# Kernel tuning notes

Measured on AMD Instinct MI355X. Metric: run time of the kernel, lower is better.

The kernel has to match this reference:

```python
import jax, jax.numpy as jnp
import numpy as np

DIM = 1024
LATENT_DIM = 512
NUM_HEADS = 16
HEAD_DIM = DIM // NUM_HEADS
SCALE = HEAD_DIM ** -0.5


def setup_inputs() -> dict:
    key = jax.random.key(0)
    k1, k2, k3, k4, k5 = jax.random.split(key, 5)
    B, xN, zN = 2, 2048, 2048
    x = jax.random.normal(k1, (B, xN, DIM), dtype=jnp.float32)
    z = jax.random.normal(k2, (B, zN, LATENT_DIM), dtype=jnp.float32)
    # torch Linear weights: [out_features, in_features]
    Wq = jax.random.normal(k3, (DIM, DIM), dtype=jnp.float32) * (DIM ** -0.5)
    Wkv = jax.random.normal(k4, (2 * DIM, LATENT_DIM), dtype=jnp.float32) * (LATENT_DIM ** -0.5)
    Wo = jax.random.normal(k5, (DIM, DIM), dtype=jnp.float32) * (DIM ** -0.5)
    return {"x": x, "z": z, "Wq": Wq, "Wkv": Wkv, "Wo": Wo}


def reference(x, z, Wq, Wkv, Wo):
    B, xN, _ = x.shape
    _, zN, _ = z.shape
    # projections (torch Linear: y = x @ W.T)
    Q = (x @ Wq.T).reshape(B, xN, NUM_HEADS, HEAD_DIM)        # [B,xN,H,D]
    KV = (z @ Wkv.T).reshape(B, zN, 2, NUM_HEADS, HEAD_DIM)   # [B,zN,2,H,D]
    K = KV[:, :, 0]                                            # [B,zN,H,D]
    V = KV[:, :, 1]
    attn = jnp.einsum('bqhd,bkhd->bhqk', Q, K) * SCALE         # [B,H,xN,zN]
    attn = jax.nn.softmax(attn, axis=-1)
    O = jnp.einsum('bhqk,bkhd->bqhd', attn, V).reshape(B, xN, DIM)
    return O @ Wo.T
```

## Files before the change

kernel.cpp:

```cpp
#include <hip/hip_runtime.h>
#include <stdint.h>

#define SEQ 2048
#define QSCALE 0.1803368801111244f
#define DEFER_THR 11.5f

typedef __attribute__((ext_vector_type(8))) short bf16x8;
typedef __attribute__((ext_vector_type(4))) short bf16x4;
typedef __attribute__((ext_vector_type(4))) float f32x4;
typedef __attribute__((ext_vector_type(16))) float f32x16;
typedef unsigned short u16;

__device__ __forceinline__ u16 f2bf(float f) {
  union { float f; uint32_t u; } v; v.f = f;
  uint32_t u = v.u;
  u += 0x7fffu + ((u >> 16) & 1u);
  return (u16)(u >> 16);
}

__device__ __forceinline__ float fast_exp2(float x) {
#if __has_builtin(__builtin_amdgcn_exp2f)
  return __builtin_amdgcn_exp2f(x);
#else
  return exp2f(x);
#endif
}

__device__ __forceinline__ uint32_t cvtpk(float a, float b) {
  uint32_t r;
  asm("v_cvt_pk_bf16_f32 %0, %1, %2" : "=v"(r) : "v"(a), "v"(b));
  return r;
}

__device__ __forceinline__ void swap_pair(uint32_t& a, uint32_t& b, int hi) {
  uint32_t ta = (uint32_t)__shfl_xor((int)a, 32);
  uint32_t tb = (uint32_t)__shfl_xor((int)b, 32);
  a = hi ? tb : a;
  b = hi ? b : ta;
}

__device__ __forceinline__ void gload_lds16(const u16* g, u16* l) {
  __builtin_amdgcn_global_load_lds((__attribute__((address_space(1))) void*)g,
                                   (__attribute__((address_space(3))) void*)l,
                                   16, 0, 0);
}

__global__ void cvt5_kernel(const float* __restrict__ x, const float* __restrict__ z,
                            const float* __restrict__ Wq, const float* __restrict__ Wkv,
                            const float* __restrict__ Wo,
                            u16* __restrict__ xb, u16* __restrict__ zb,
                            u16* __restrict__ wqb, u16* __restrict__ wkvb,
                            u16* __restrict__ wob) {
  const int X4 = 1048576, Z4 = 524288, W4 = 262144;
  const int total = X4 + Z4 + 3 * W4;
  int i = blockIdx.x * blockDim.x + threadIdx.x;
  const int stride = gridDim.x * blockDim.x;
  for (; i < total; i += stride) {
    const float* src; u16* dst; int j = i;
    if (j < X4)              { src = x;   dst = xb; }
    else if ((j -= X4) < Z4) { src = z;   dst = zb; }
    else if ((j -= Z4) < W4) { src = Wq;  dst = wqb; }
    else if ((j -= W4) < W4) { src = Wkv; dst = wkvb; }
    else       { j -= W4;      src = Wo;  dst = wob; }
    float4 v = ((const float4*)src)[j];
    bf16x4 o;
    o[0] = (short)f2bf(v.x); o[1] = (short)f2bf(v.y);
    o[2] = (short)f2bf(v.z); o[3] = (short)f2bf(v.w);
    ((bf16x4*)dst)[j] = o;
  }
}

template <int BN, typename CT>
__device__ __forceinline__ void gemm_bt_body(const u16* __restrict__ A,
                                             const u16* __restrict__ B,
                                             CT* __restrict__ C,
                                             int N, int K, float scale,
                                             int tm, int tn, u16* As, u16* Bs) {
  constexpr int NB = BN / 32;
  constexpr int NBG = BN / 64;
  const int tid = threadIdx.x;
  const int wid = tid >> 6;
  const int lane = tid & 63;
  const int lg = lane >> 4, lq = lane & 15;
  const int wr = wid >> 1, wc = wid & 1;

  f32x4 acc[4][NB];
#pragma unroll
  for (int m = 0; m < 4; m++)
#pragma unroll
    for (int n = 0; n < NB; n++)
#pragma unroll
      for (int e = 0; e < 4; e++) acc[m][n][e] = 0.f;

  const int r0 = tid >> 2;
  const int s0 = tid & 3;
  const int sc = (s0 ^ ((r0 >> 1) & 3)) * 8;
  const u16* gA0 = A + (size_t)(tm * 128 + r0) * K + sc;
  const u16* gA1 = gA0 + (size_t)64 * K;
  const u16* gB0 = B + (size_t)(tn * BN + r0) * K + sc;
  const u16* gB1 = gB0 + (size_t)64 * K;
  u16* lA = As + wid * 512;
  u16* lB = Bs + wid * 512;

  const int rslot = (lg ^ ((lq >> 1) & 3)) * 8;

  for (int k0 = 0; k0 < K; k0 += 32) {
    __syncthreads();
    gload_lds16(gA0 + k0, lA);
    gload_lds16(gA1 + k0, lA + 2048);
    gload_lds16(gB0 + k0, lB);
    if constexpr (NBG == 2) gload_lds16(gB1 + k0, lB + 2048);
    __syncthreads();

    bf16x8 af[4], bfr[NB];
#pragma unroll
    for (int m = 0; m < 4; m++)
      af[m] = *(const bf16x8*)(As + (wr * 64 + m * 16 + lq) * 32 + rslot);
#pragma unroll
    for (int n = 0; n < NB; n++)
      bfr[n] = *(const bf16x8*)(Bs + (wc * (BN / 2) + n * 16 + lq) * 32 + rslot);
#pragma unroll
    for (int m = 0; m < 4; m++)
#pragma unroll
      for (int n = 0; n < NB; n++)
        acc[m][n] = __builtin_amdgcn_mfma_f32_16x16x32_bf16(af[m], bfr[n], acc[m][n], 0, 0, 0);
  }

#pragma unroll
  for (int m = 0; m < 4; m++) {
    const int row = tm * 128 + wr * 64 + m * 16 + lg * 4;
#pragma unroll
    for (int i = 0; i < 4; i++) {
      CT* cp = C + (size_t)(row + i) * N + tn * BN + wc * (BN / 2) + lq;
#pragma unroll
      for (int n = 0; n < NB; n++) {
        float v = acc[m][n][i] * scale;
        if constexpr (sizeof(CT) == 2) cp[n * 16] = (CT)f2bf(v);
        else                            cp[n * 16] = (CT)v;
      }
    }
  }
}

__global__ __launch_bounds__(256) void qkv_gemm(const u16* __restrict__ xb,
                                                const u16* __restrict__ zb,
                                                const u16* __restrict__ Wqb,
                                                const u16* __restrict__ Wkvb,
                                                u16* __restrict__ Qb,
                                                u16* __restrict__ Kb,
                                                u16* __restrict__ VTb) {
  __shared__ __align__(16) u16 As[128 * 32];
  __shared__ __align__(16) u16 Bs[128 * 32];
  int g = blockIdx.x;
  if (g < 256) {
    gemm_bt_body<128, u16>(xb, Wqb, Qb, 1024, 1024, QSCALE, g >> 3, g & 7, As, Bs);
  } else if (g < 512) {
    g -= 256;
    gemm_bt_body<128, u16>(zb, Wkvb, Kb, 1024, 512, 1.f, g >> 3, g & 7, As, Bs);
  } else {
    g -= 512;
    gemm_bt_body<128, u16>(Wkvb + 1024 * 512, zb, VTb, 4096, 512, 1.f, g >> 5, g & 31, As, Bs);
  }
}

__global__ __launch_bounds__(256) void o_gemm(const u16* __restrict__ Ob,
                                              const u16* __restrict__ Wob,
                                              float* __restrict__ out) {
  __shared__ __align__(16) u16 As[128 * 32];
  __shared__ __align__(16) u16 Bs[64 * 32];
  gemm_bt_body<64, float>(Ob, Wob, out, 1024, 1024, 1.f, blockIdx.y, blockIdx.x, As, Bs);
}

__global__ __launch_bounds__(256, 4) void attn_kernel(const u16* __restrict__ Q,
                                                      const u16* __restrict__ K,
                                                      const u16* __restrict__ VT,
                                                      u16* __restrict__ OP,
                                                      float2* __restrict__ ml) {
  __shared__ __align__(16) u16 LDS[16384];

  const int tid = threadIdx.x;
  const int wid = tid >> 6;
  const int lane = tid & 63;
  const int l31 = lane & 31;
  const int hi = lane >> 5;

  const int bi = blockIdx.x;
  const int xcd = bi & 7, j = bi >> 3;
  const int qt = j & 15;
  const int s  = (j >> 4) & 1;
  const int bh = xcd + 8 * (j >> 5);
  const int b = bh >> 4, h = bh & 15;
  const int t0 = s * 16;

  const int q0 = qt * 128 + wid * 32;

  bf16x8 qf[4];
  {
    const u16* qp = Q + (size_t)(b * SEQ + q0 + l31) * 1024 + h * 64 + hi * 8;
#pragma unroll
    for (int ks = 0; ks < 4; ks++) qf[ks] = *(const bf16x8*)(qp + ks * 16);
  }

  f32x16 of[2];
#pragma unroll
  for (int d = 0; d < 2; d++)
#pragma unroll
    for (int e = 0; e < 16; e++) of[d][e] = 0.f;
  float m_run = -3.0e38f, l_run = 0.f;

  const char* rdB[4];
#pragma unroll
  for (int ks = 0; ks < 4; ks++)
    rdB[ks] = (const char*)LDS + l31 * 128 + ((((2 * ks + hi) ^ (lane & 7))) << 4);

  const int r0 = tid >> 3;
  const int srcc = ((tid & 7) ^ (r0 & 7)) << 3;
  const u16* gK = K + (size_t)(b * SEQ + r0) * 1024 + h * 64 + srcc;
  const u16* gV = VT + (size_t)(h * 64 + r0) * 4096 + b * SEQ + srcc;
  u16* lK = LDS + wid * 512;
  u16* lV = LDS + 8192 + wid * 512;

  auto stage = [&](int t, int buf) {
    const u16* sk = gK + (size_t)t * 64 * 1024;
    gload_lds16(sk, lK + buf * 4096);
    gload_lds16(sk + (size_t)32 * 1024, lK + buf * 4096 + 2048);
    const u16* sv = gV + t * 64;
    gload_lds16(sv, lV + buf * 4096);
    gload_lds16(sv + (size_t)32 * 4096, lV + buf * 4096 + 2048);
  };

  auto tile_compute = [&](int buf) {
    const int bo = buf * 8192;

    f32x16 sacc[2];
#pragma unroll
    for (int kb = 0; kb < 2; kb++)
#pragma unroll
      for (int e = 0; e < 16; e++) sacc[kb][e] = 0.f;
    __builtin_amdgcn_s_setprio(1);
#pragma unroll
    for (int kb = 0; kb < 2; kb++)
#pragma unroll
      for (int ks = 0; ks < 4; ks++) {
        bf16x8 kf = *(const bf16x8*)(rdB[ks] + bo + kb * 4096);
        sacc[kb] = __builtin_amdgcn_mfma_f32_32x32x16_bf16(kf, qf[ks], sacc[kb], 0, 0, 0);
      }
    __builtin_amdgcn_s_setprio(0);

    float a0 = sacc[0][0], a1 = sacc[0][1], a2 = sacc[0][2], a3 = sacc[0][3];
#pragma unroll
    for (int e = 4; e < 16; e += 4) {
      a0 = fmaxf(a0, sacc[0][e]);     a1 = fmaxf(a1, sacc[0][e + 1]);
      a2 = fmaxf(a2, sacc[0][e + 2]); a3 = fmaxf(a3, sacc[0][e + 3]);
    }
#pragma unroll
    for (int e = 0; e < 16; e += 4) {
      a0 = fmaxf(a0, sacc[1][e]);     a1 = fmaxf(a1, sacc[1][e + 1]);
      a2 = fmaxf(a2, sacc[1][e + 2]); a3 = fmaxf(a3, sacc[1][e + 3]);
    }
    float tmax = fmaxf(fmaxf(a0, a1), fmaxf(a2, a3));
    tmax = fmaxf(tmax, __shfl_xor(tmax, 32));

    if (!__all(tmax <= m_run + DEFER_THR)) {
      const float m_new = fmaxf(m_run, tmax);
      const float esc = fast_exp2(m_run - m_new);
      l_run *= esc;
#pragma unroll
      for (int r = 0; r < 16; r++) {
        const int qof = (r & 3) + 8 * (r >> 2) + 4 * hi;
        const float e = __shfl(esc, qof);
        of[0][r] *= e;
        of[1][r] *= e;
      }
      m_run = m_new;
    }

    float s0 = 0.f, s1 = 0.f, s2 = 0.f, s3 = 0.f;
#pragma unroll
    for (int kb = 0; kb < 2; kb++)
#pragma unroll
      for (int e = 0; e < 16; e += 4) {
        float p0 = fast_exp2(sacc[kb][e] - m_run);
        float p1 = fast_exp2(sacc[kb][e + 1] - m_run);
        float p2 = fast_exp2(sacc[kb][e + 2] - m_run);
        float p3 = fast_exp2(sacc[kb][e + 3] - m_run);
        sacc[kb][e] = p0; sacc[kb][e + 1] = p1; sacc[kb][e + 2] = p2; sacc[kb][e + 3] = p3;
        s0 += p0; s1 += p1; s2 += p2; s3 += p3;
      }
    l_run += (s0 + s1) + (s2 + s3);

    bf16x8 pa[4];
#pragma unroll
    for (int kb = 0; kb < 2; kb++) {
      uint32_t c0 = cvtpk(sacc[kb][0],  sacc[kb][1]);
      uint32_t c1 = cvtpk(sacc[kb][2],  sacc[kb][3]);
      uint32_t c2 = cvtpk(sacc[kb][4],  sacc[kb][5]);
      uint32_t c3 = cvtpk(sacc[kb][6],  sacc[kb][7]);
      uint32_t c4 = cvtpk(sacc[kb][8],  sacc[kb][9]);
      uint32_t c5 = cvtpk(sacc[kb][10], sacc[kb][11]);
      uint32_t c6 = cvtpk(sacc[kb][12], sacc[kb][13]);
      uint32_t c7 = cvtpk(sacc[kb][14], sacc[kb][15]);
      swap_pair(c0, c2, hi);
      swap_pair(c1, c3, hi);
      swap_pair(c4, c6, hi);
      swap_pair(c5, c7, hi);
      union { bf16x8 v; uint32_t d[4]; } u0, u1;
      u0.d[0] = c0; u0.d[1] = c1; u0.d[2] = c2; u0.d[3] = c3;
      u1.d[0] = c4; u1.d[1] = c5; u1.d[2] = c6; u1.d[3] = c7;
      pa[2 * kb] = u0.v;
      pa[2 * kb + 1] = u1.v;
    }

    __builtin_amdgcn_s_setprio(1);
#pragma unroll
    for (int ks = 0; ks < 4; ks++)
#pragma unroll
      for (int db = 0; db < 2; db++) {
        bf16x8 vf = *(const bf16x8*)(rdB[ks] + bo + 16384 + db * 4096);
        of[db] = __builtin_amdgcn_mfma_f32_32x32x16_bf16(pa[ks], vf, of[db], 0, 0, 0);
      }
    __builtin_amdgcn_s_setprio(0);
  };

  stage(t0, 0);
  __syncthreads();
#pragma unroll 1
  for (int tt = 0; tt < 16; tt += 2) {
    stage(t0 + tt + 1, 1);
    tile_compute(0);
    __syncthreads();
    if (tt < 14) stage(t0 + tt + 2, 0);
    tile_compute(1);
    __syncthreads();
  }

  const float lsum = l_run + __shfl_xor(l_run, 32);
  const float linv = 1.f / lsum;

  u16* OPs = OP + (size_t)s * 4096 * 1024;
#pragma unroll
  for (int r = 0; r < 16; r++) {
    const int qof = (r & 3) + 8 * (r >> 2) + 4 * hi;
    const float li = __shfl(linv, qof);
    u16* op = OPs + (size_t)(b * SEQ + q0 + qof) * 1024 + h * 64 + l31;
    op[0]  = f2bf(of[0][r] * li);
    op[32] = f2bf(of[1][r] * li);
  }
  if (hi == 0) {
    const int grow = b * SEQ + q0 + l31;
    ml[s * (4096 * 16) + grow * 16 + h] = make_float2(m_run, lsum);
  }
}

__global__ __launch_bounds__(256) void combine_kernel(const u16* __restrict__ OP,
                                                      const float2* __restrict__ ml,
                                                      u16* __restrict__ Ob) {
  const int i = blockIdx.x * 256 + threadIdx.x;
  const int grow = i >> 7;
  const int h = (i >> 3) & 15;
  const float2 a0 = ml[grow * 16 + h];
  const float2 a1 = ml[4096 * 16 + grow * 16 + h];
  const float M = fmaxf(a0.x, a1.x);
  float w0 = a0.y * fast_exp2(a0.x - M);
  float w1 = a1.y * fast_exp2(a1.x - M);
  const float inv = 1.f / (w0 + w1);
  w0 *= inv; w1 *= inv;
  const bf16x8 p0 = ((const bf16x8*)OP)[i];
  const bf16x8 p1 = ((const bf16x8*)(OP + (size_t)4096 * 1024))[i];
  bf16x8 o;
#pragma unroll
  for (int e = 0; e < 8; e++) {
    union { uint32_t u; float f; } f0, f1;
    f0.u = ((uint32_t)(u16)p0[e]) << 16;
    f1.u = ((uint32_t)(u16)p1[e]) << 16;
    o[e] = (short)f2bf(w0 * f0.f + w1 * f1.f);
  }
  ((bf16x8*)Ob)[i] = o;
}

extern "C" void kernel_launch(void* const* d_in, const int* in_sizes, int n_in,
                              void* d_out, int out_size, void* d_ws, size_t ws_size,
                              hipStream_t stream) {
  const float* x   = (const float*)d_in[0];
  const float* z   = (const float*)d_in[1];
  const float* Wq  = (const float*)d_in[2];
  const float* Wkv = (const float*)d_in[3];
  const float* Wo  = (const float*)d_in[4];
  float* out = (float*)d_out;

  char* ws = (char*)d_ws;
  const size_t MB = 1024ull * 1024ull;
  u16* xb   = (u16*)(ws + 0);
  u16* zb   = (u16*)(ws + 8 * MB);
  u16* Wqb  = (u16*)(ws + 12 * MB);
  u16* Wkvb = (u16*)(ws + 14 * MB);
  u16* Wob  = (u16*)(ws + 16 * MB);
  u16* Qb   = (u16*)(ws + 18 * MB);
  u16* Kb   = (u16*)(ws + 26 * MB);
  u16* VTb  = (u16*)(ws + 34 * MB);
  u16* Ob   = (u16*)(ws + 42 * MB);
  u16* OP   = (u16*)(ws + 0);
  float2* ml = (float2*)(ws + 50 * MB);

  cvt5_kernel<<<2048, 256, 0, stream>>>(x, z, Wq, Wkv, Wo, xb, zb, Wqb, Wkvb, Wob);

  qkv_gemm<<<768, 256, 0, stream>>>(xb, zb, Wqb, Wkvb, Qb, Kb, VTb);

  attn_kernel<<<1024, 256, 0, stream>>>(Qb, Kb, VTb, OP, ml);

  combine_kernel<<<2048, 256, 0, stream>>>(OP, ml, Ob);

  o_gemm<<<dim3(16, 32), 256, 0, stream>>>(Ob, Wob, out);
}
```

Before: 121.8 us.

## Deepen GEMM K-step to 64 with 8-slot XOR swizzle and XCD-aware block mapping

The shared GEMM body now stages 64-wide K slices per iteration instead of 32, with a matching 8-way XOR swizzle on the LDS tiles. That halves the number of barrier pairs per tile and issues two MFMA sub-steps between syncs. The QKV and output GEMMs also remap block indices so that blocks sharing operand rows land on the same XCD, aiming for better L2 reuse. The cost is doubled LDS per block, with an occupancy hint of 3 set on the QKV kernel; moving combine_kernel is only code reordering.

After: 117.5 us. 3.5% less time.

```diff
diff --git a/kernel.cpp b/kernel.cpp
--- a/kernel.cpp
+++ b/kernel.cpp
@@ -71,13 +71,12 @@
 }
 
 template <int BN, typename CT>
-__device__ __forceinline__ void gemm_bt_body(const u16* __restrict__ A,
-                                             const u16* __restrict__ B,
-                                             CT* __restrict__ C,
-                                             int N, int K, float scale,
-                                             int tm, int tn, u16* As, u16* Bs) {
+__device__ __forceinline__ void gemm64_body(const u16* __restrict__ A,
+                                            const u16* __restrict__ B,
+                                            CT* __restrict__ C,
+                                            int N, int K, float scale,
+                                            int tm, int tn, u16* As, u16* Bs) {
   constexpr int NB = BN / 32;
-  constexpr int NBG = BN / 64;
   const int tid = threadIdx.x;
   const int wid = tid >> 6;
   const int lane = tid & 63;
@@ -92,38 +91,40 @@
 #pragma unroll
       for (int e = 0; e < 4; e++) acc[m][n][e] = 0.f;
 
-  const int r0 = tid >> 2;
-  const int s0 = tid & 3;
-  const int sc = (s0 ^ ((r0 >> 1) & 3)) * 8;
-  const u16* gA0 = A + (size_t)(tm * 128 + r0) * K + sc;
-  const u16* gA1 = gA0 + (size_t)64 * K;
-  const u16* gB0 = B + (size_t)(tn * BN + r0) * K + sc;
-  const u16* gB1 = gB0 + (size_t)64 * K;
+  const int r0 = tid >> 3;
+  const int c0 = tid & 7;
+  const int sc = (c0 ^ (r0 & 7)) * 8;
+  const u16* gA = A + (size_t)(tm * 128 + r0) * K + sc;
+  const u16* gB = B + (size_t)(tn * BN + r0) * K + sc;
   u16* lA = As + wid * 512;
   u16* lB = Bs + wid * 512;
 
-  const int rslot = (lg ^ ((lq >> 1) & 3)) * 8;
-
-  for (int k0 = 0; k0 < K; k0 += 32) {
+  for (int k0 = 0; k0 < K; k0 += 64) {
     __syncthreads();
-    gload_lds16(gA0 + k0, lA);
-    gload_lds16(gA1 + k0, lA + 2048);
-    gload_lds16(gB0 + k0, lB);
-    if constexpr (NBG == 2) gload_lds16(gB1 + k0, lB + 2048);
+#pragma unroll
+    for (int i = 0; i < 4; i++)
+      gload_lds16(gA + k0 + (size_t)(32 * i) * K, lA + i * 2048);
+#pragma unroll
+    for (int i = 0; i < NB; i++)
+      gload_lds16(gB + k0 + (size_t)(32 * i) * K, lB + i * 2048);
     __syncthreads();
 
-    bf16x8 af[4], bfr[NB];
-#pragma unroll
-    for (int m = 0; m < 4; m++)
-      af[m] = *(const bf16x8*)(As + (wr * 64 + m * 16 + lq) * 32 + rslot);
-#pragma unroll
-    for (int n = 0; n < NB; n++)
-      bfr[n] = *(const bf16x8*)(Bs + (wc * (BN / 2) + n * 16 + lq) * 32 + rslot);
-#pragma unroll
-    for (int m = 0; m < 4; m++)
+#pragma unroll
+    for (int ks = 0; ks < 2; ks++) {
+      const int slot = ((ks * 4 + lg) ^ (lq & 7)) * 8;
+      bf16x8 af[4], bfr[NB];
+#pragma unroll
+      for (int m = 0; m < 4; m++)
+        af[m] = *(const bf16x8*)(As + (wr * 64 + m * 16 + lq) * 64 + slot);
 #pragma unroll
       for (int n = 0; n < NB; n++)
-        acc[m][n] = __builtin_amdgcn_mfma_f32_16x16x32_bf16(af[m], bfr[n], acc[m][n], 0, 0, 0);
+        bfr[n] = *(const bf16x8*)(Bs + (wc * (BN / 2) + n * 16 + lq) * 64 + slot);
+#pragma unroll
+      for (int m = 0; m < 4; m++)
+#pragma unroll
+        for (int n = 0; n < NB; n++)
+          acc[m][n] = __builtin_amdgcn_mfma_f32_16x16x32_bf16(af[m], bfr[n], acc[m][n], 0, 0, 0);
+    }
   }
 
 #pragma unroll
@@ -142,33 +143,64 @@
   }
 }
 
-__global__ __launch_bounds__(256) void qkv_gemm(const u16* __restrict__ xb,
-                                                const u16* __restrict__ zb,
-                                                const u16* __restrict__ Wqb,
-                                                const u16* __restrict__ Wkvb,
-                                                u16* __restrict__ Qb,
-                                                u16* __restrict__ Kb,
-                                                u16* __restrict__ VTb) {
-  __shared__ __align__(16) u16 As[128 * 32];
-  __shared__ __align__(16) u16 Bs[128 * 32];
-  int g = blockIdx.x;
+__global__ __launch_bounds__(256, 3) void qkv_gemm(const u16* __restrict__ xb,
+                                                   const u16* __restrict__ zb,
+                                                   const u16* __restrict__ Wqb,
+                                                   const u16* __restrict__ Wkvb,
+                                                   u16* __restrict__ Qb,
+                                                   u16* __restrict__ Kb,
+                                                   u16* __restrict__ VTb) {
+  __shared__ __align__(16) u16 As[128 * 64];
+  __shared__ __align__(16) u16 Bs[128 * 64];
+  const int bi = blockIdx.x;
+  int g = (bi & 7) * 96 + (bi >> 3);
   if (g < 256) {
-    gemm_bt_body<128, u16>(xb, Wqb, Qb, 1024, 1024, QSCALE, g >> 3, g & 7, As, Bs);
+    gemm64_body<128, u16>(xb, Wqb, Qb, 1024, 1024, QSCALE, g >> 3, g & 7, As, Bs);
   } else if (g < 512) {
     g -= 256;
-    gemm_bt_body<128, u16>(zb, Wkvb, Kb, 1024, 512, 1.f, g >> 3, g & 7, As, Bs);
+    gemm64_body<128, u16>(zb, Wkvb, Kb, 1024, 512, 1.f, g >> 3, g & 7, As, Bs);
   } else {
     g -= 512;
-    gemm_bt_body<128, u16>(Wkvb + 1024 * 512, zb, VTb, 4096, 512, 1.f, g >> 5, g & 31, As, Bs);
-  }
+    gemm64_body<128, u16>(Wkvb + 1024 * 512, zb, VTb, 4096, 512, 1.f, g >> 5, g & 31, As, Bs);
+  }
+}
+
+__global__ __launch_bounds__(256) void combine_kernel(const u16* __restrict__ OP,
+                                                      const float2* __restrict__ ml,
+                                                      u16* __restrict__ Ob) {
+  const int i = blockIdx.x * 256 + threadIdx.x;
+  const int grow = i >> 7;
+  const int h = (i >> 3) & 15;
+  const float2 a0 = ml[grow * 16 + h];
+  const float2 a1 = ml[4096 * 16 + grow * 16 + h];
+  const float M = fmaxf(a0.x, a1.x);
+  float w0 = a0.y * fast_exp2(a0.x - M);
+  float w1 = a1.y * fast_exp2(a1.x - M);
+  const float inv = 1.f / (w0 + w1);
+  w0 *= inv; w1 *= inv;
+  const bf16x8 p0 = ((const bf16x8*)OP)[i];
+  const bf16x8 p1 = ((const bf16x8*)(OP + (size_t)4096 * 1024))[i];
+  bf16x8 o;
+#pragma unroll
+  for (int e = 0; e < 8; e++) {
+    union { uint32_t u; float f; } f0, f1;
+    f0.u = ((uint32_t)(u16)p0[e]) << 16;
+    f1.u = ((uint32_t)(u16)p1[e]) << 16;
+    o[e] = (short)f2bf(w0 * f0.f + w1 * f1.f);
+  }
+  ((bf16x8*)Ob)[i] = o;
 }
 
 __global__ __launch_bounds__(256) void o_gemm(const u16* __restrict__ Ob,
                                               const u16* __restrict__ Wob,
                                               float* __restrict__ out) {
-  __shared__ __align__(16) u16 As[128 * 32];
-  __shared__ __align__(16) u16 Bs[64 * 32];
-  gemm_bt_body<64, float>(Ob, Wob, out, 1024, 1024, 1.f, blockIdx.y, blockIdx.x, As, Bs);
+  __shared__ __align__(16) u16 As[128 * 64];
+  __shared__ __align__(16) u16 Bs[64 * 64];
+  const int bi = blockIdx.x;
+  const int xcd = bi & 7, j = bi >> 3;
+  const int tm = xcd * 4 + (j >> 4);
+  const int tn = j & 15;
+  gemm64_body<64, float>(Ob, Wob, out, 1024, 1024, 1.f, tm, tn, As, Bs);
 }
 
 __global__ __launch_bounds__(256, 4) void attn_kernel(const u16* __restrict__ Q,
@@ -352,32 +384,6 @@
   }
 }
 
-__global__ __launch_bounds__(256) void combine_kernel(const u16* __restrict__ OP,
-                                                      const float2* __restrict__ ml,
-                                                      u16* __restrict__ Ob) {
-  const int i = blockIdx.x * 256 + threadIdx.x;
-  const int grow = i >> 7;
-  const int h = (i >> 3) & 15;
-  const float2 a0 = ml[grow * 16 + h];
-  const float2 a1 = ml[4096 * 16 + grow * 16 + h];
-  const float M = fmaxf(a0.x, a1.x);
-  float w0 = a0.y * fast_exp2(a0.x - M);
-  float w1 = a1.y * fast_exp2(a1.x - M);
-  const float inv = 1.f / (w0 + w1);
-  w0 *= inv; w1 *= inv;
-  const bf16x8 p0 = ((const bf16x8*)OP)[i];
-  const bf16x8 p1 = ((const bf16x8*)(OP + (size_t)4096 * 1024))[i];
-  bf16x8 o;
-#pragma unroll
-  for (int e = 0; e < 8; e++) {
-    union { uint32_t u; float f; } f0, f1;
-    f0.u = ((uint32_t)(u16)p0[e]) << 16;
-    f1.u = ((uint32_t)(u16)p1[e]) << 16;
-    o[e] = (short)f2bf(w0 * f0.f + w1 * f1.f);
-  }
-  ((bf16x8*)Ob)[i] = o;
-}
-
 extern "C" void kernel_launch(void* const* d_in, const int* in_sizes, int n_in,
                               void* d_out, int out_size, void* d_ws, size_t ws_size,
                               hipStream_t stream) {
@@ -410,5 +416,5 @@
 
   combine_kernel<<<2048, 256, 0, stream>>>(OP, ml, Ob);
 
-  o_gemm<<<dim3(16, 32), 256, 0, stream>>>(Ob, Wob, out);
-}
+  o_gemm<<<512, 256, 0, stream>>>(Ob, Wob, out);
+}
```
